# Optimization experiments

Measured on AMD Instinct MI355X. Metric: run time of the kernel, lower is better.

The kernel has to match this reference:

```python
import jax, jax.numpy as jnp
import numpy as np

E = 768           # EMBEDDING_DIM
L = 768           # LATENT_DIM
H = 12            # ATTENTION_HEAD_COUNT
HD = L // H       # head_dim = 64
EPS = 1e-5


def _linear_params(key, fan_in, fan_out):
    kw, kb = jax.random.split(key)
    bound = 1.0 / np.sqrt(fan_in)
    w = jax.random.uniform(kw, (fan_in, fan_out), jnp.float32, -bound, bound)
    b = jax.random.uniform(kb, (fan_out,), jnp.float32, -bound, bound)
    return w, b


def layer_norm(x, g, b):
    m = jnp.mean(x, axis=-1, keepdims=True)
    v = jnp.mean((x - m) ** 2, axis=-1, keepdims=True)
    return (x - m) * jax.lax.rsqrt(v + EPS) * g + b


def setup_inputs() -> dict:
    key = jax.random.key(0)
    ks = jax.random.split(key, 8)
    B, N, M = 8, 1024, 1024
    x = jax.random.normal(ks[0], (B, N, E), jnp.float32)
    y = jax.random.normal(ks[1], (B, M, E), jnp.float32)
    wq, bq = _linear_params(ks[2], E, L)
    wk, bk = _linear_params(ks[3], E, L)
    wv, bv = _linear_params(ks[4], E, E * H)
    w_in, b_in = _linear_params(ks[5], E, L)
    w_out, b_out = _linear_params(ks[6], L, E)
    ones = jnp.ones((E,), jnp.float32)
    zeros = jnp.zeros((E,), jnp.float32)
    return {
        'x': x, 'y': y,
        'ln1_g': ones, 'ln1_b': zeros,
        'ln2_g': ones, 'ln2_b': zeros,
        'ln3_g': ones, 'ln3_b': zeros,
        'wq': wq, 'bq': bq,
        'wk': wk, 'bk': bk,
        'wv': wv, 'bv': bv,
        'w_in': w_in, 'b_in': b_in,
        'w_out': w_out, 'b_out': b_out,
    }


def reference(x, y, ln1_g, ln1_b, ln2_g, ln2_b, ln3_g, ln3_b,
              wq, bq, wk, bk, wv, bv, w_in, b_in, w_out, b_out):
    B, N, _ = x.shape
    M = y.shape[1]
    xn = layer_norm(x, ln1_g, ln1_b)
    yn = layer_norm(y, ln2_g, ln2_b)
    # projections; per-head value dim is the FULL embedding dim (non-standard)
    q = (xn @ wq + bq).reshape(B, N, H, HD)        # bnhd
    k = (yn @ wk + bk).reshape(B, M, H, HD)        # bmhd
    v = (yn @ wv + bv).reshape(B, M, H, E)         # bmhe
    a = jnp.einsum('bnhd,bmhd->bhnm', q, k) / jnp.sqrt(jnp.float32(HD))
    a = jax.nn.softmax(a, axis=-1)
    # attention output fused with the sum over heads (heads summed, not concat)
    dx = jnp.einsum('bhnm,bmhe->bne', a, v)
    h = xn + dx
    h = layer_norm(h, ln3_g, ln3_b)
    mlp = jax.nn.relu(h @ w_in + b_in) @ w_out + b_out
    return (h + mlp, yn)
```

## Files before the change

kernel.cpp:

```cpp
#include <hip/hip_runtime.h>
#include <hip/hip_bf16.h>
#include <stdint.h>

typedef __bf16 bf16_t;
typedef __bf16 bf16x8 __attribute__((ext_vector_type(8)));
typedef float  f32x4  __attribute__((ext_vector_type(4)));

typedef __attribute__((address_space(3))) unsigned int lds_u32;
typedef const __attribute__((address_space(1))) unsigned int glob_u32;
#define GLDS16(g, l) __builtin_amdgcn_global_load_lds((glob_u32*)(g), (lds_u32*)(l), 16, 0, 0)

__device__ __forceinline__ f32x4 mfma16(bf16x8 a, bf16x8 b, f32x4 c) {
    return __builtin_amdgcn_mfma_f32_16x16x32_bf16(a, b, c, 0, 0, 0);
}

__device__ __forceinline__ float ldv(const void* p, long i, int fp32mode) {
    return fp32mode ? ((const float*)p)[i] : (float)((const bf16_t*)p)[i];
}

__global__ __launch_bounds__(256)
void detect_dtype(const void* __restrict__ x, int* __restrict__ flag) {
    __shared__ int cnt;
    if (threadIdx.x == 0) cnt = 0;
    __syncthreads();
    const bf16_t* p = (const bf16_t*)x;
    int local = 0;
    for (int i = threadIdx.x; i < 4096; i += 256) {
        const float v = (float)p[i];
        if (!(fabsf(v) < 1e6f)) local++;
    }
    atomicAdd(&cnt, local);
    __syncthreads();
    if (threadIdx.x == 0) { flag[0] = (cnt >= 16) ? 1 : 0; flag[1] = 0; }
}

__global__ __launch_bounds__(256)
void transpose_cvt(const void* __restrict__ in, bf16_t* __restrict__ out,
                   int R, int C, const int* __restrict__ flagp) {
    __shared__ bf16_t t[32][33];
    const int mode = *flagp;
    const long zi = (long)blockIdx.z * R * C;
    const int c0 = blockIdx.x * 32;
    const int r0 = blockIdx.y * 32;
    const int x  = threadIdx.x;
    const int y0 = threadIdx.y;
    for (int yy = y0; yy < 32; yy += 8)
        t[yy][x] = (bf16_t)ldv(in, zi + (long)(r0 + yy) * C + c0 + x, mode);
    __syncthreads();
    for (int yy = y0; yy < 32; yy += 8)
        out[zi + (long)(c0 + yy) * R + r0 + x] = t[x][yy];
}

__global__ __launch_bounds__(256)
void transpose_wv(const void* __restrict__ in, bf16_t* __restrict__ out,
                  const int* __restrict__ flagp) {
    __shared__ bf16_t t[32][33];
    const int mode = *flagp;
    const int h  = blockIdx.z;
    const int e0 = blockIdx.x * 32;
    const int k0 = blockIdx.y * 32;
    const int x  = threadIdx.x;
    const int y0 = threadIdx.y;
    for (int yy = y0; yy < 32; yy += 8)
        t[yy][x] = (bf16_t)ldv(in, (long)(k0 + yy) * 9216 + h * 768 + e0 + x, mode);
    __syncthreads();
    for (int yy = y0; yy < 32; yy += 8)
        out[(long)(e0 + yy) * 9216 + h * 768 + k0 + x] = t[x][yy];
}

__global__ __launch_bounds__(256)
void bvsum_k(const void* __restrict__ bv, float* __restrict__ out,
             const int* __restrict__ flagp) {
    const int mode = *flagp;
    const int e = blockIdx.x * 256 + threadIdx.x;
    if (e < 768) {
        float s = 0.f;
#pragma unroll
        for (int h = 0; h < 12; ++h) s += ldv(bv, h * 768 + e, mode);
        out[e] = s;
    }
}

__global__ __launch_bounds__(256)
void ln768(const void* __restrict__ in, bf16_t* __restrict__ out,
           const void* __restrict__ gam, const void* __restrict__ bet,
           const int* __restrict__ dmodep, const int* __restrict__ pmodep) {
    __shared__ float rs[256], rq[256];
    const int dm = *dmodep, pm = *pmodep;
    const long base = (long)blockIdx.x * 768;
    const int tid = threadIdx.x;
    float v[3];
    float s = 0.f, q = 0.f;
#pragma unroll
    for (int i = 0; i < 3; ++i) {
        v[i] = ldv(in, base + i * 256 + tid, dm);
        s += v[i];
        q += v[i] * v[i];
    }
    rs[tid] = s; rq[tid] = q;
    __syncthreads();
    for (int st = 128; st > 0; st >>= 1) {
        if (tid < st) { rs[tid] += rs[tid + st]; rq[tid] += rq[tid + st]; }
        __syncthreads();
    }
    const float mean = rs[0] * (1.0f / 768.0f);
    const float var  = rq[0] * (1.0f / 768.0f) - mean * mean;
    const float rstd = rsqrtf(var + 1e-5f);
#pragma unroll
    for (int i = 0; i < 3; ++i) {
        const int c = i * 256 + tid;
        out[base + c] = (bf16_t)((v[i] - mean) * rstd * ldv(gam, c, pm) + ldv(bet, c, pm));
    }
}

__device__ __forceinline__ void kloop64(const bf16_t* Az, const bf16_t* Bz,
                                        int K, int lda, int ldb, int tid,
                                        char* As, char* Bs,
                                        int wn, int l15, int quad,
                                        f32x4 (&acc)[4][2]) {
    const int srow = tid >> 3;
    const int sc   = ((tid & 7) * 16) ^ ((srow & 7) << 4);
    char* lA = As + (tid >> 6) * 1024;
    char* lB = Bs + (tid >> 6) * 1024;
    const int rsw = (l15 & 7) << 4;
    for (int k0 = 0; k0 < K; k0 += 64) {
        __syncthreads();
        GLDS16((const char*)(Az + (long)srow * lda + k0) + sc, lA);
        GLDS16((const char*)(Az + (long)(srow + 32) * lda + k0) + sc, lA + 4096);
#pragma unroll
        for (int p = 0; p < 4; ++p)
            GLDS16((const char*)(Bz + (long)(srow + p * 32) * ldb + k0) + sc, lB + p * 4096);
        __syncthreads();
#pragma unroll
        for (int kk = 0; kk < 64; kk += 32) {
            bf16x8 af[4], bfr[2];
            const int cb = kk * 2 + quad * 16;
#pragma unroll
            for (int i = 0; i < 4; ++i)
                af[i] = *(const bf16x8*)(As + (i * 16 + l15) * 128 + (cb ^ rsw));
#pragma unroll
            for (int j = 0; j < 2; ++j)
                bfr[j] = *(const bf16x8*)(Bs + (wn + j * 16 + l15) * 128 + (cb ^ rsw));
#pragma unroll
            for (int i = 0; i < 4; ++i)
#pragma unroll
                for (int j = 0; j < 2; ++j)
                    acc[i][j] = mfma16(af[i], bfr[j], acc[i][j]);
        }
    }
}

__device__ __forceinline__ int xcd_swz(int lin, int nwg) {
    return (lin & 7) * (nwg >> 3) + (lin >> 3);
}

__global__ __launch_bounds__(256)
void gemm_bt(const bf16_t* __restrict__ A, const bf16_t* __restrict__ B,
             bf16_t* __restrict__ C,
             int K, int lda, int ldb, int ldc,
             const void* __restrict__ bias, const int* __restrict__ flagp,
             const bf16_t* __restrict__ res, int do_relu) {
    __shared__ char As[64 * 128];
    __shared__ char Bs[128 * 128];
    const int bmode = *flagp;
    const int swz = xcd_swz(blockIdx.y * 6 + blockIdx.x, 768);
    const int n0 = (swz % 6) * 128;
    const int m0 = (swz / 6) * 64;
    const bf16_t* Az = A + (long)m0 * lda;
    const bf16_t* Bz = B + (long)n0 * ldb;

    const int tid  = threadIdx.x;
    const int lane = tid & 63;
    const int wn   = (tid >> 6) * 32;
    const int l15  = lane & 15;
    const int quad = lane >> 4;

    const f32x4 fz = {0.f, 0.f, 0.f, 0.f};
    f32x4 acc[4][2];
#pragma unroll
    for (int i = 0; i < 4; ++i)
#pragma unroll
        for (int j = 0; j < 2; ++j) acc[i][j] = fz;

    kloop64(Az, Bz, K, lda, ldb, tid, As, Bs, wn, l15, quad, acc);

#pragma unroll
    for (int i = 0; i < 4; ++i) {
#pragma unroll
        for (int j = 0; j < 2; ++j) {
            const int mb = m0 + i * 16 + quad * 4;
            const int nc = n0 + wn + j * 16 + l15;
#pragma unroll
            for (int r = 0; r < 4; ++r) {
                float v = acc[i][j][r];
                if (bias) v += ldv(bias, nc, bmode);
                if (do_relu) v = fmaxf(v, 0.0f);
                if (res) v += (float)res[(long)(mb + r) * ldc + nc];
                C[(long)(mb + r) * ldc + nc] = (bf16_t)v;
            }
        }
    }
}

__global__ __launch_bounds__(256)
void gemm_qk(const bf16_t* __restrict__ xn, const bf16_t* __restrict__ ynb,
             const bf16_t* __restrict__ wqT, const bf16_t* __restrict__ wkT,
             bf16_t* __restrict__ qb, bf16_t* __restrict__ kb,
             const void* __restrict__ bq, const void* __restrict__ bk,
             const int* __restrict__ flagp) {
    __shared__ char As[64 * 128];
    __shared__ char Bs[128 * 128];
    const int bmode = *flagp;
    const int z = blockIdx.z;
    const bf16_t* A = z ? ynb : xn;
    const bf16_t* B = z ? wkT : wqT;
    bf16_t*       C = z ? kb  : qb;
    const void* bias = z ? bk : bq;
    const int swz = xcd_swz(blockIdx.y * 6 + blockIdx.x, 768);
    const int n0 = (swz % 6) * 128;
    const int m0 = (swz / 6) * 64;
    const bf16_t* Az = A + (long)m0 * 768;
    const bf16_t* Bz = B + (long)n0 * 768;

    const int tid  = threadIdx.x;
    const int lane = tid & 63;
    const int wn   = (tid >> 6) * 32;
    const int l15  = lane & 15;
    const int quad = lane >> 4;

    const f32x4 fz = {0.f, 0.f, 0.f, 0.f};
    f32x4 acc[4][2];
#pragma unroll
    for (int i = 0; i < 4; ++i)
#pragma unroll
        for (int j = 0; j < 2; ++j) acc[i][j] = fz;

    kloop64(Az, Bz, 768, 768, 768, tid, As, Bs, wn, l15, quad, acc);

#pragma unroll
    for (int i = 0; i < 4; ++i) {
#pragma unroll
        for (int j = 0; j < 2; ++j) {
            const int mb = m0 + i * 16 + quad * 4;
            const int nc = n0 + wn + j * 16 + l15;
#pragma unroll
            for (int r = 0; r < 4; ++r)
                C[(long)(mb + r) * 768 + nc] = (bf16_t)(acc[i][j][r] + ldv(bias, nc, bmode));
        }
    }
}

__global__ __launch_bounds__(256)
void gemm_vt(const bf16_t* __restrict__ W2T, const bf16_t* __restrict__ ynb,
             bf16_t* __restrict__ VTc, int h0, int ldP) {
    __shared__ char As[64 * 128];
    __shared__ char Bs[128 * 128];
    const int b   = blockIdx.x;
    const int hc  = blockIdx.z;
    const int e0  = (blockIdx.y >> 3) * 64;
    const int mc0 = (blockIdx.y & 7) * 128;
    const bf16_t* Az = W2T + (long)e0 * 9216 + (h0 + hc) * 768;
    const bf16_t* Bz = ynb + ((long)b * 1024 + mc0) * 768;

    const int tid  = threadIdx.x;
    const int lane = tid & 63;
    const int wn   = (tid >> 6) * 32;
    const int l15  = lane & 15;
    const int quad = lane >> 4;

    const f32x4 fz = {0.f, 0.f, 0.f, 0.f};
    f32x4 acc[4][2];
#pragma unroll
    for (int i = 0; i < 4; ++i)
#pragma unroll
        for (int j = 0; j < 2; ++j) acc[i][j] = fz;

    kloop64(Az, Bz, 768, 9216, 768, tid, As, Bs, wn, l15, quad, acc);

    bf16_t* C = VTc + (long)b * 768 * ldP + (long)hc * 1024;
#pragma unroll
    for (int i = 0; i < 4; ++i) {
#pragma unroll
        for (int j = 0; j < 2; ++j) {
            const int er = e0 + i * 16 + quad * 4;
            const int mc = mc0 + wn + j * 16 + l15;
#pragma unroll
            for (int r = 0; r < 4; ++r)
                C[(long)(er + r) * ldP + mc] = (bf16_t)acc[i][j][r];
        }
    }
}

__global__ __launch_bounds__(256)
void gemm_dx(const bf16_t* __restrict__ P, const bf16_t* __restrict__ VTc,
             float* __restrict__ dxf, const bf16_t* __restrict__ xnb,
             const float* __restrict__ bvs, bf16_t* __restrict__ hp,
             int KK, int ldP, int mode) {
    __shared__ char As[64 * 128];
    __shared__ char Bs[128 * 128];
    const int b  = blockIdx.x;
    const int t  = blockIdx.y;
    const int m0 = (t / 6) * 64;
    const int n0 = (t % 6) * 128;
    const bf16_t* Az = P   + ((long)b * 1024 + m0) * ldP;
    const bf16_t* Bz = VTc + ((long)b * 768  + n0) * ldP;

    const int tid  = threadIdx.x;
    const int lane = tid & 63;
    const int wn   = (tid >> 6) * 32;
    const int l15  = lane & 15;
    const int quad = lane >> 4;

    const f32x4 fz = {0.f, 0.f, 0.f, 0.f};
    f32x4 acc[4][2];
#pragma unroll
    for (int i = 0; i < 4; ++i)
#pragma unroll
        for (int j = 0; j < 2; ++j) acc[i][j] = fz;

    kloop64(Az, Bz, KK, ldP, ldP, tid, As, Bs, wn, l15, quad, acc);

#pragma unroll
    for (int i = 0; i < 4; ++i) {
#pragma unroll
        for (int j = 0; j < 2; ++j) {
            const int gr = b * 1024 + m0 + i * 16 + quad * 4;
            const int nc = n0 + wn + j * 16 + l15;
#pragma unroll
            for (int r = 0; r < 4; ++r) {
                const long gi = (long)(gr + r) * 768 + nc;
                float v = acc[i][j][r];
                if (mode == 1 || mode == 2) v += dxf[gi];
                if (mode <= 1) dxf[gi] = v;
                else hp[gi] = (bf16_t)(v + bvs[nc] + (float)xnb[gi]);
            }
        }
    }
}

__global__ __launch_bounds__(512, 8)
void fused_S(const bf16_t* __restrict__ Q, const bf16_t* __restrict__ Kp,
             bf16_t* __restrict__ P, int h0, int ldP) {
    __shared__ bf16_t Pl[16][1032];
    __shared__ float  rmax[8][16];
    __shared__ float  rsum[8][16];

    const int bx   = blockIdx.x;
    const int b    = bx & 7;
    const int n0   = ((bx >> 3) & 63) * 16;
    const int hc   = bx >> 9;
    const int h    = h0 + hc;
    const int tid  = threadIdx.x;
    const int w    = tid >> 6;
    const int lane = tid & 63;
    const int l15  = lane & 15;
    const int quad = lane >> 4;

    const f32x4 fz = {0.f, 0.f, 0.f, 0.f};
    const long qoff = (long)(b * 1024 + n0 + l15) * 768 + h * 64 + quad * 8;
    const long koff = (long)(b * 1024) * 768 + h * 64 + quad * 8;

    f32x4 s[8];
#pragma unroll
    for (int f = 0; f < 8; ++f) s[f] = fz;
    const bf16x8 qa0 = *(const bf16x8*)(Q + qoff);
    const bf16x8 qa1 = *(const bf16x8*)(Q + qoff + 32);
#pragma unroll
    for (int f = 0; f < 8; ++f) {
        const int m = w * 128 + f * 16 + l15;
        const bf16_t* kp = Kp + koff + (long)m * 768;
        s[f] = mfma16(qa0, *(const bf16x8*)kp, s[f]);
        s[f] = mfma16(qa1, *(const bf16x8*)(kp + 32), s[f]);
    }
    float rm[4] = {-3e38f, -3e38f, -3e38f, -3e38f};
#pragma unroll
    for (int f = 0; f < 8; ++f)
#pragma unroll
        for (int r = 0; r < 4; ++r) {
            s[f][r] *= 0.125f;
            rm[r] = fmaxf(rm[r], s[f][r]);
        }
#pragma unroll
    for (int off = 1; off < 16; off <<= 1)
#pragma unroll
        for (int r = 0; r < 4; ++r) rm[r] = fmaxf(rm[r], __shfl_xor(rm[r], off));
    if (l15 == 0) {
#pragma unroll
        for (int r = 0; r < 4; ++r) rmax[w][quad * 4 + r] = rm[r];
    }
    __syncthreads();
    float gm[4];
#pragma unroll
    for (int r = 0; r < 4; ++r) {
        float mx = rmax[0][quad * 4 + r];
#pragma unroll
        for (int w2 = 1; w2 < 8; ++w2) mx = fmaxf(mx, rmax[w2][quad * 4 + r]);
        gm[r] = mx;
    }
    float ps[4] = {0.f, 0.f, 0.f, 0.f};
#pragma unroll
    for (int f = 0; f < 8; ++f)
#pragma unroll
        for (int r = 0; r < 4; ++r) {
            const float p = __expf(s[f][r] - gm[r]);
            s[f][r] = p;
            ps[r] += p;
        }
#pragma unroll
    for (int off = 1; off < 16; off <<= 1)
#pragma unroll
        for (int r = 0; r < 4; ++r) ps[r] += __shfl_xor(ps[r], off);
    if (l15 == 0) {
#pragma unroll
        for (int r = 0; r < 4; ++r) rsum[w][quad * 4 + r] = ps[r];
    }
    __syncthreads();
#pragma unroll
    for (int r = 0; r < 4; ++r) {
        float ss = 0.f;
#pragma unroll
        for (int w2 = 0; w2 < 8; ++w2) ss += rsum[w2][quad * 4 + r];
        gm[r] = 1.0f / ss;
    }
#pragma unroll
    for (int f = 0; f < 8; ++f)
#pragma unroll
        for (int r = 0; r < 4; ++r)
            Pl[quad * 4 + r][w * 128 + f * 16 + l15] = (bf16_t)(s[f][r] * gm[r]);
    __syncthreads();

    const long pbase = ((long)b * 1024 + n0) * ldP + (long)hc * 1024;
    const int rr = tid >> 5;
    const int c0 = (tid & 31) * 32;
    bf16_t* dst = P + pbase + (long)rr * ldP + c0;
#pragma unroll
    for (int u = 0; u < 4; ++u)
        *(bf16x8*)(dst + u * 8) = *(const bf16x8*)(&Pl[rr][c0 + u * 8]);
}

__global__ __launch_bounds__(256)
void emit2(const bf16_t* __restrict__ a, const bf16_t* __restrict__ b,
           void* __restrict__ out, const int* __restrict__ flagp) {
    const int mode = *flagp;
    const long n = 6291456;
    const long stride = (long)gridDim.x * blockDim.x;
    for (long i = (long)blockIdx.x * blockDim.x + threadIdx.x; i < 2 * n; i += stride) {
        const bf16_t v = (i < n) ? a[i] : b[i - n];
        if (mode) ((float*)out)[i] = (float)v;
        else      ((bf16_t*)out)[i] = v;
    }
}

extern "C" void kernel_launch(void* const* d_in, const int* in_sizes, int n_in,
                              void* d_out, int out_size, void* d_ws, size_t ws_size,
                              hipStream_t stream) {
    (void)in_sizes; (void)n_in; (void)out_size;

    const void* x    = d_in[0];
    const void* y    = d_in[1];
    const void* ln1g = d_in[2];
    const void* ln1b = d_in[3];
    const void* ln2g = d_in[4];
    const void* ln2b = d_in[5];
    const void* ln3g = d_in[6];
    const void* ln3b = d_in[7];
    const void* wq   = d_in[8];
    const void* bq   = d_in[9];
    const void* wk   = d_in[10];
    const void* bk   = d_in[11];
    const void* wv   = d_in[12];
    const void* bv   = d_in[13];
    const void* wi   = d_in[14];
    const void* bi   = d_in[15];
    const void* wo   = d_in[16];
    const void* bo   = d_in[17];

    char* ws = (char*)d_ws;
    bf16_t* xn    = (bf16_t*)(ws + 0);
    bf16_t* ynb   = (bf16_t*)(ws + 12582912);
    bf16_t* qb    = (bf16_t*)(ws + 25165824);
    bf16_t* kb    = (bf16_t*)(ws + 37748736);
    bf16_t* W2T   = (bf16_t*)(ws + 50331648);
    bf16_t* wqT   = (bf16_t*)(ws + 64487424);
    bf16_t* wkT   = (bf16_t*)(ws + 65667072);
    bf16_t* wiT   = (bf16_t*)(ws + 66846720);
    bf16_t* woT   = (bf16_t*)(ws + 68026368);
    float*  bvs   = (float*) (ws + 69206016);
    int*    flag  = (int*)   (ws + 69210112);
    float*  dxf   = (float*) (ws + 69214208);

    static const int GS[5] = {12, 6, 4, 3, 2};
    int G = 2;
    for (int i = 0; i < 5; ++i) {
        const unsigned long long need =
            96215040ULL + (unsigned long long)GS[i] * 29360128ULL;
        if (need <= (unsigned long long)ws_size) { G = GS[i]; break; }
    }
    const int KK  = G * 1024;
    const int ldP = KK + 64;
    bf16_t* Pcat = (bf16_t*)(ws + 94380032);
    bf16_t* VTc  = Pcat + (size_t)8192 * ldP;
    bf16_t* hpre = qb;
    bf16_t* hn   = kb;
    bf16_t* mid  = Pcat;
    bf16_t* res0 = xn;
    const int* F = flag;
    const int* Z = flag + 1;

    detect_dtype<<<1, 256, 0, stream>>>(x, flag);

    const dim3 tb(32, 8);
    transpose_cvt<<<dim3(24, 24, 1), tb, 0, stream>>>(wq, wqT, 768, 768, F);
    transpose_cvt<<<dim3(24, 24, 1), tb, 0, stream>>>(wk, wkT, 768, 768, F);
    transpose_cvt<<<dim3(24, 24, 1), tb, 0, stream>>>(wi, wiT, 768, 768, F);
    transpose_cvt<<<dim3(24, 24, 1), tb, 0, stream>>>(wo, woT, 768, 768, F);
    transpose_wv<<<dim3(24, 24, 12), tb, 0, stream>>>(wv, W2T, F);
    bvsum_k<<<3, 256, 0, stream>>>(bv, bvs, F);

    ln768<<<8192, 256, 0, stream>>>(x, xn, ln1g, ln1b, F, F);
    ln768<<<8192, 256, 0, stream>>>(y, ynb, ln2g, ln2b, F, F);

    gemm_qk<<<dim3(6, 128, 2), 256, 0, stream>>>(xn, ynb, wqT, wkT, qb, kb, bq, bk, F);

    const int npass = 12 / G;
    for (int p = 0; p < npass; ++p) {
        const int h0 = p * G;
        fused_S<<<512 * G, 512, 0, stream>>>(qb, kb, Pcat, h0, ldP);
        gemm_vt<<<dim3(8, 96, G), 256, 0, stream>>>(W2T, ynb, VTc, h0, ldP);
        const int mode = (npass == 1) ? 3 : (p == 0 ? 0 : (p == npass - 1 ? 2 : 1));
        gemm_dx<<<dim3(8, 96), 256, 0, stream>>>(Pcat, VTc, dxf, xn, bvs, hpre,
                                                 KK, ldP, mode);
    }

    ln768<<<8192, 256, 0, stream>>>(hpre, hn, ln3g, ln3b, Z, F);

    gemm_bt<<<dim3(6, 128), 256, 0, stream>>>(hn, wiT, mid, 768, 768, 768, 768,
                                              bi, F, nullptr, 1);
    gemm_bt<<<dim3(6, 128), 256, 0, stream>>>(mid, woT, res0, 768, 768, 768, 768,
                                              bo, F, hn, 0);

    emit2<<<2048, 256, 0, stream>>>(res0, ynb, d_out, F);
}
```

Before: 841.9 us.

## Use 128x128 tiles for value GEMMs and split-K the dx GEMM

Adds a 128x128 K-loop in which each of the four waves owns a 64x64 sub-tile. The V-transpose and attention-output GEMMs now use it instead of the 64x128 tile, which raises data reuse per LDS load. The dx GEMM is split into two K halves written to separate fp32 buffers, which keeps the grid large enough to fill the device. A new elementwise kernel sums the halves and adds the bias and residual. This costs a larger workspace and an extra pass over fp32 memory.

New measurement: 969.2 us. 1.15x slower.

```diff
diff --git a/kernel.cpp b/kernel.cpp
--- a/kernel.cpp
+++ b/kernel.cpp
@@ -145,6 +145,43 @@
             for (int i = 0; i < 4; ++i)
 #pragma unroll
                 for (int j = 0; j < 2; ++j)
+                    acc[i][j] = mfma16(af[i], bfr[j], acc[i][j]);
+        }
+    }
+}
+
+__device__ __forceinline__ void kloop128(const bf16_t* Az, const bf16_t* Bz,
+                                         int K, int lda, int ldb, int tid,
+                                         char* As, char* Bs,
+                                         int wm, int wn, int l15, int quad,
+                                         f32x4 (&acc)[4][4]) {
+    const int srow = tid >> 3;
+    const int sc   = ((tid & 7) * 16) ^ ((srow & 7) << 4);
+    char* lA = As + (tid >> 6) * 1024;
+    char* lB = Bs + (tid >> 6) * 1024;
+    const int rsw = (l15 & 7) << 4;
+    for (int k0 = 0; k0 < K; k0 += 64) {
+        __syncthreads();
+#pragma unroll
+        for (int p = 0; p < 4; ++p) {
+            GLDS16((const char*)(Az + (long)(srow + p * 32) * lda + k0) + sc, lA + p * 4096);
+            GLDS16((const char*)(Bz + (long)(srow + p * 32) * ldb + k0) + sc, lB + p * 4096);
+        }
+        __syncthreads();
+#pragma unroll
+        for (int kk = 0; kk < 64; kk += 32) {
+            bf16x8 af[4], bfr[4];
+            const int cb = kk * 2 + quad * 16;
+#pragma unroll
+            for (int i = 0; i < 4; ++i)
+                af[i] = *(const bf16x8*)(As + (wm + i * 16 + l15) * 128 + (cb ^ rsw));
+#pragma unroll
+            for (int j = 0; j < 4; ++j)
+                bfr[j] = *(const bf16x8*)(Bs + (wn + j * 16 + l15) * 128 + (cb ^ rsw));
+#pragma unroll
+            for (int i = 0; i < 4; ++i)
+#pragma unroll
+                for (int j = 0; j < 4; ++j)
                     acc[i][j] = mfma16(af[i], bfr[j], acc[i][j]);
         }
     }
@@ -253,36 +290,38 @@
 __global__ __launch_bounds__(256)
 void gemm_vt(const bf16_t* __restrict__ W2T, const bf16_t* __restrict__ ynb,
              bf16_t* __restrict__ VTc, int h0, int ldP) {
-    __shared__ char As[64 * 128];
+    __shared__ char As[128 * 128];
     __shared__ char Bs[128 * 128];
     const int b   = blockIdx.x;
     const int hc  = blockIdx.z;
-    const int e0  = (blockIdx.y >> 3) * 64;
+    const int e0  = (blockIdx.y >> 3) * 128;
     const int mc0 = (blockIdx.y & 7) * 128;
     const bf16_t* Az = W2T + (long)e0 * 9216 + (h0 + hc) * 768;
     const bf16_t* Bz = ynb + ((long)b * 1024 + mc0) * 768;
 
     const int tid  = threadIdx.x;
     const int lane = tid & 63;
-    const int wn   = (tid >> 6) * 32;
+    const int w    = tid >> 6;
+    const int wm   = (w >> 1) * 64;
+    const int wn   = (w & 1) * 64;
     const int l15  = lane & 15;
     const int quad = lane >> 4;
 
     const f32x4 fz = {0.f, 0.f, 0.f, 0.f};
-    f32x4 acc[4][2];
+    f32x4 acc[4][4];
 #pragma unroll
     for (int i = 0; i < 4; ++i)
 #pragma unroll
-        for (int j = 0; j < 2; ++j) acc[i][j] = fz;
-
-    kloop64(Az, Bz, 768, 9216, 768, tid, As, Bs, wn, l15, quad, acc);
+        for (int j = 0; j < 4; ++j) acc[i][j] = fz;
+
+    kloop128(Az, Bz, 768, 9216, 768, tid, As, Bs, wm, wn, l15, quad, acc);
 
     bf16_t* C = VTc + (long)b * 768 * ldP + (long)hc * 1024;
 #pragma unroll
     for (int i = 0; i < 4; ++i) {
 #pragma unroll
-        for (int j = 0; j < 2; ++j) {
-            const int er = e0 + i * 16 + quad * 4;
+        for (int j = 0; j < 4; ++j) {
+            const int er = e0 + wm + i * 16 + quad * 4;
             const int mc = mc0 + wn + j * 16 + l15;
 #pragma unroll
             for (int r = 0; r < 4; ++r)
@@ -293,49 +332,58 @@
 
 __global__ __launch_bounds__(256)
 void gemm_dx(const bf16_t* __restrict__ P, const bf16_t* __restrict__ VTc,
-             float* __restrict__ dxf, const bf16_t* __restrict__ xnb,
-             const float* __restrict__ bvs, bf16_t* __restrict__ hp,
-             int KK, int ldP, int mode) {
-    __shared__ char As[64 * 128];
+             float* __restrict__ dxf, int KH, int ldP, int first) {
+    __shared__ char As[128 * 128];
     __shared__ char Bs[128 * 128];
     const int b  = blockIdx.x;
     const int t  = blockIdx.y;
-    const int m0 = (t / 6) * 64;
+    const int ks = blockIdx.z;
+    const int m0 = (t / 6) * 128;
     const int n0 = (t % 6) * 128;
-    const bf16_t* Az = P   + ((long)b * 1024 + m0) * ldP;
-    const bf16_t* Bz = VTc + ((long)b * 768  + n0) * ldP;
+    const bf16_t* Az = P   + ((long)b * 1024 + m0) * ldP + ks * KH;
+    const bf16_t* Bz = VTc + ((long)b * 768  + n0) * ldP + ks * KH;
+    float* dxs = dxf + (long)ks * 6291456;
 
     const int tid  = threadIdx.x;
     const int lane = tid & 63;
-    const int wn   = (tid >> 6) * 32;
+    const int w    = tid >> 6;
+    const int wm   = (w >> 1) * 64;
+    const int wn   = (w & 1) * 64;
     const int l15  = lane & 15;
     const int quad = lane >> 4;
 
     const f32x4 fz = {0.f, 0.f, 0.f, 0.f};
-    f32x4 acc[4][2];
+    f32x4 acc[4][4];
 #pragma unroll
     for (int i = 0; i < 4; ++i)
 #pragma unroll
-        for (int j = 0; j < 2; ++j) acc[i][j] = fz;
-
-    kloop64(Az, Bz, KK, ldP, ldP, tid, As, Bs, wn, l15, quad, acc);
+        for (int j = 0; j < 4; ++j) acc[i][j] = fz;
+
+    kloop128(Az, Bz, KH, ldP, ldP, tid, As, Bs, wm, wn, l15, quad, acc);
 
 #pragma unroll
     for (int i = 0; i < 4; ++i) {
 #pragma unroll
-        for (int j = 0; j < 2; ++j) {
-            const int gr = b * 1024 + m0 + i * 16 + quad * 4;
+        for (int j = 0; j < 4; ++j) {
+            const int gr = b * 1024 + m0 + wm + i * 16 + quad * 4;
             const int nc = n0 + wn + j * 16 + l15;
 #pragma unroll
             for (int r = 0; r < 4; ++r) {
                 const long gi = (long)(gr + r) * 768 + nc;
                 float v = acc[i][j][r];
-                if (mode == 1 || mode == 2) v += dxf[gi];
-                if (mode <= 1) dxf[gi] = v;
-                else hp[gi] = (bf16_t)(v + bvs[nc] + (float)xnb[gi]);
+                if (!first) v += dxs[gi];
+                dxs[gi] = v;
             }
         }
     }
+}
+
+__global__ __launch_bounds__(256)
+void hpre_ep(const float* __restrict__ dxf, const float* __restrict__ bvs,
+             const bf16_t* __restrict__ xn, bf16_t* __restrict__ hp) {
+    const long i = (long)blockIdx.x * 256 + threadIdx.x;
+    const int e = (int)(i % 768);
+    hp[i] = (bf16_t)(dxf[i] + dxf[i + 6291456] + bvs[e] + (float)xn[i]);
 }
 
 __global__ __launch_bounds__(512, 8)
@@ -493,12 +541,12 @@
     int G = 2;
     for (int i = 0; i < 5; ++i) {
         const unsigned long long need =
-            96215040ULL + (unsigned long long)GS[i] * 29360128ULL;
+            121380864ULL + (unsigned long long)GS[i] * 29360128ULL;
         if (need <= (unsigned long long)ws_size) { G = GS[i]; break; }
     }
     const int KK  = G * 1024;
     const int ldP = KK + 64;
-    bf16_t* Pcat = (bf16_t*)(ws + 94380032);
+    bf16_t* Pcat = (bf16_t*)(ws + 119545856);
     bf16_t* VTc  = Pcat + (size_t)8192 * ldP;
     bf16_t* hpre = qb;
     bf16_t* hn   = kb;
@@ -526,11 +574,12 @@
     for (int p = 0; p < npass; ++p) {
         const int h0 = p * G;
         fused_S<<<512 * G, 512, 0, stream>>>(qb, kb, Pcat, h0, ldP);
-        gemm_vt<<<dim3(8, 96, G), 256, 0, stream>>>(W2T, ynb, VTc, h0, ldP);
-        const int mode = (npass == 1) ? 3 : (p == 0 ? 0 : (p == npass - 1 ? 2 : 1));
-        gemm_dx<<<dim3(8, 96), 256, 0, stream>>>(Pcat, VTc, dxf, xn, bvs, hpre,
-                                                 KK, ldP, mode);
-    }
+        gemm_vt<<<dim3(8, 48, G), 256, 0, stream>>>(W2T, ynb, VTc, h0, ldP);
+        gemm_dx<<<dim3(8, 48, 2), 256, 0, stream>>>(Pcat, VTc, dxf, KK / 2, ldP,
+                                                    p == 0);
+    }
+
+    hpre_ep<<<24576, 256, 0, stream>>>(dxf, bvs, xn, hpre);
 
     ln768<<<8192, 256, 0, stream>>>(hpre, hn, ln3g, ln3b, Z, F);
 
```

## Fuse output emission into final GEMM and LayerNorm, merge transpose and LN launches

Applied to the files above, without the earlier changes.

Removes the separate emit kernel by having the last MLP GEMM write the first output directly (in fp32 or bf16) and having the y LayerNorm also write its result into the second output slot. Merges the two input LayerNorm launches into one grid and the four square weight transposes into one launch. This cuts a full extra read/write pass over both outputs plus several launch overheads, at the cost of more branching inside the kernels.

After: 823.3 us. 1.02x faster.

```diff
diff --git a/kernel.cpp b/kernel.cpp
--- a/kernel.cpp
+++ b/kernel.cpp
@@ -35,20 +35,25 @@
 }
 
 __global__ __launch_bounds__(256)
-void transpose_cvt(const void* __restrict__ in, bf16_t* __restrict__ out,
-                   int R, int C, const int* __restrict__ flagp) {
+void transpose_w4(const void* __restrict__ i0, const void* __restrict__ i1,
+                  const void* __restrict__ i2, const void* __restrict__ i3,
+                  bf16_t* __restrict__ o0, bf16_t* __restrict__ o1,
+                  bf16_t* __restrict__ o2, bf16_t* __restrict__ o3,
+                  const int* __restrict__ flagp) {
     __shared__ bf16_t t[32][33];
     const int mode = *flagp;
-    const long zi = (long)blockIdx.z * R * C;
+    const int z = blockIdx.z;
+    const void* in = (z == 0) ? i0 : (z == 1) ? i1 : (z == 2) ? i2 : i3;
+    bf16_t*    out = (z == 0) ? o0 : (z == 1) ? o1 : (z == 2) ? o2 : o3;
     const int c0 = blockIdx.x * 32;
     const int r0 = blockIdx.y * 32;
-    const int x  = threadIdx.x;
-    const int y0 = threadIdx.y;
+    const int x  = threadIdx.x & 31;
+    const int y0 = threadIdx.x >> 5;
     for (int yy = y0; yy < 32; yy += 8)
-        t[yy][x] = (bf16_t)ldv(in, zi + (long)(r0 + yy) * C + c0 + x, mode);
+        t[yy][x] = (bf16_t)ldv(in, (long)(r0 + yy) * 768 + c0 + x, mode);
     __syncthreads();
     for (int yy = y0; yy < 32; yy += 8)
-        out[zi + (long)(c0 + yy) * R + r0 + x] = t[x][yy];
+        out[(long)(c0 + yy) * 768 + r0 + x] = t[x][yy];
 }
 
 __global__ __launch_bounds__(256)
@@ -78,6 +83,54 @@
 #pragma unroll
         for (int h = 0; h < 12; ++h) s += ldv(bv, h * 768 + e, mode);
         out[e] = s;
+    }
+}
+
+__global__ __launch_bounds__(256)
+void ln_xy(const void* __restrict__ x, const void* __restrict__ y,
+           bf16_t* __restrict__ xn, bf16_t* __restrict__ ynb,
+           const void* __restrict__ g1, const void* __restrict__ b1,
+           const void* __restrict__ g2, const void* __restrict__ b2,
+           void* __restrict__ outp, const int* __restrict__ flagp) {
+    __shared__ float rs[256], rq[256];
+    const int mode = *flagp;
+    const int ri   = blockIdx.x;
+    const int isy  = ri >> 13;
+    const long rr  = ri & 8191;
+    const void* in = isy ? y : x;
+    const void* gam = isy ? g2 : g1;
+    const void* bet = isy ? b2 : b1;
+    const long base = rr * 768;
+    const int tid = threadIdx.x;
+    float v[3];
+    float s = 0.f, q = 0.f;
+#pragma unroll
+    for (int i = 0; i < 3; ++i) {
+        v[i] = ldv(in, base + i * 256 + tid, mode);
+        s += v[i];
+        q += v[i] * v[i];
+    }
+    rs[tid] = s; rq[tid] = q;
+    __syncthreads();
+    for (int st = 128; st > 0; st >>= 1) {
+        if (tid < st) { rs[tid] += rs[tid + st]; rq[tid] += rq[tid + st]; }
+        __syncthreads();
+    }
+    const float mean = rs[0] * (1.0f / 768.0f);
+    const float var  = rq[0] * (1.0f / 768.0f) - mean * mean;
+    const float rstd = rsqrtf(var + 1e-5f);
+    bf16_t* dst = isy ? ynb : xn;
+#pragma unroll
+    for (int i = 0; i < 3; ++i) {
+        const int c = i * 256 + tid;
+        const float o = (v[i] - mean) * rstd * ldv(gam, c, mode) + ldv(bet, c, mode);
+        const bf16_t ob = (bf16_t)o;
+        dst[base + c] = ob;
+        if (isy) {
+            const long oi = 6291456 + base + c;
+            if (mode) ((float*)outp)[oi] = (float)ob;
+            else      ((bf16_t*)outp)[oi] = ob;
+        }
     }
 }
 
@@ -159,7 +212,8 @@
              bf16_t* __restrict__ C,
              int K, int lda, int ldb, int ldc,
              const void* __restrict__ bias, const int* __restrict__ flagp,
-             const bf16_t* __restrict__ res, int do_relu) {
+             const bf16_t* __restrict__ res, int do_relu,
+             void* __restrict__ eout) {
     __shared__ char As[64 * 128];
     __shared__ char Bs[128 * 128];
     const int bmode = *flagp;
@@ -196,7 +250,13 @@
                 if (bias) v += ldv(bias, nc, bmode);
                 if (do_relu) v = fmaxf(v, 0.0f);
                 if (res) v += (float)res[(long)(mb + r) * ldc + nc];
-                C[(long)(mb + r) * ldc + nc] = (bf16_t)v;
+                const long gi = (long)(mb + r) * ldc + nc;
+                if (eout) {
+                    if (bmode) ((float*)eout)[gi] = v;
+                    else       ((bf16_t*)eout)[gi] = (bf16_t)v;
+                } else {
+                    C[gi] = (bf16_t)v;
+                }
             }
         }
     }
@@ -438,19 +498,6 @@
         *(bf16x8*)(dst + u * 8) = *(const bf16x8*)(&Pl[rr][c0 + u * 8]);
 }
 
-__global__ __launch_bounds__(256)
-void emit2(const bf16_t* __restrict__ a, const bf16_t* __restrict__ b,
-           void* __restrict__ out, const int* __restrict__ flagp) {
-    const int mode = *flagp;
-    const long n = 6291456;
-    const long stride = (long)gridDim.x * blockDim.x;
-    for (long i = (long)blockIdx.x * blockDim.x + threadIdx.x; i < 2 * n; i += stride) {
-        const bf16_t v = (i < n) ? a[i] : b[i - n];
-        if (mode) ((float*)out)[i] = (float)v;
-        else      ((bf16_t*)out)[i] = v;
-    }
-}
-
 extern "C" void kernel_launch(void* const* d_in, const int* in_sizes, int n_in,
                               void* d_out, int out_size, void* d_ws, size_t ws_size,
                               hipStream_t stream) {
@@ -503,22 +550,18 @@
     bf16_t* hpre = qb;
     bf16_t* hn   = kb;
     bf16_t* mid  = Pcat;
-    bf16_t* res0 = xn;
     const int* F = flag;
     const int* Z = flag + 1;
 
     detect_dtype<<<1, 256, 0, stream>>>(x, flag);
 
-    const dim3 tb(32, 8);
-    transpose_cvt<<<dim3(24, 24, 1), tb, 0, stream>>>(wq, wqT, 768, 768, F);
-    transpose_cvt<<<dim3(24, 24, 1), tb, 0, stream>>>(wk, wkT, 768, 768, F);
-    transpose_cvt<<<dim3(24, 24, 1), tb, 0, stream>>>(wi, wiT, 768, 768, F);
-    transpose_cvt<<<dim3(24, 24, 1), tb, 0, stream>>>(wo, woT, 768, 768, F);
-    transpose_wv<<<dim3(24, 24, 12), tb, 0, stream>>>(wv, W2T, F);
+    transpose_w4<<<dim3(24, 24, 4), 256, 0, stream>>>(wq, wk, wi, wo,
+                                                      wqT, wkT, wiT, woT, F);
+    transpose_wv<<<dim3(24, 24, 12), dim3(32, 8), 0, stream>>>(wv, W2T, F);
     bvsum_k<<<3, 256, 0, stream>>>(bv, bvs, F);
 
-    ln768<<<8192, 256, 0, stream>>>(x, xn, ln1g, ln1b, F, F);
-    ln768<<<8192, 256, 0, stream>>>(y, ynb, ln2g, ln2b, F, F);
+    ln_xy<<<16384, 256, 0, stream>>>(x, y, xn, ynb, ln1g, ln1b, ln2g, ln2b,
+                                     d_out, F);
 
     gemm_qk<<<dim3(6, 128, 2), 256, 0, stream>>>(xn, ynb, wqT, wkT, qb, kb, bq, bk, F);
 
@@ -535,9 +578,7 @@
     ln768<<<8192, 256, 0, stream>>>(hpre, hn, ln3g, ln3b, Z, F);
 
     gemm_bt<<<dim3(6, 128), 256, 0, stream>>>(hn, wiT, mid, 768, 768, 768, 768,
-                                              bi, F, nullptr, 1);
-    gemm_bt<<<dim3(6, 128), 256, 0, stream>>>(mid, woT, res0, 768, 768, 768, 768,
-                                              bo, F, hn, 0);
-
-    emit2<<<2048, 256, 0, stream>>>(res0, ynb, d_out, F);
-}
+                                              bi, F, nullptr, 1, nullptr);
+    gemm_bt<<<dim3(6, 128), 256, 0, stream>>>(mid, woT, nullptr, 768, 768, 768, 768,
+                                              bo, F, hn, 0, d_out);
+}
```
